# Kernel tuning notes

Measured on AMD Instinct MI355X. Metric: run time of the kernel, lower is better.

## Reference

```python
import jax, jax.numpy as jnp
import numpy as np


def setup_inputs() -> dict:
    key = jax.random.key(0)
    k_in, k_w = jax.random.split(key)
    input = jax.random.normal(k_in, (16, 64, 64, 512), dtype=jnp.float32)
    weight = jax.random.normal(k_w, (512, 512), dtype=jnp.float32)
    return {"input": input, "weight": weight}


def reference(input, weight):
    # Faithful to the torch source, including its quirky (weight*weight).sum(0)
    # (sum over the vocab axis -> (embed_dim,) vector, broadcast over vocab
    # columns; valid here because vocab_size == embed_dim).
    batch_dims, embed_dim = input.shape[:-1], input.shape[-1]
    x = input.reshape(-1, embed_dim)                     # (N, D)
    dists = -2.0 * jnp.einsum("nd,vd->nv", x, weight) + jnp.sum(weight * weight, axis=0)[None, :]
    idxes = jnp.argmin(dists, axis=1)                    # (N,)
    values = weight[idxes].reshape(*batch_dims, embed_dim)
    return values
```

## Files before the change

### kernel.cpp

```cpp
#include <hip/hip_runtime.h>


#define DIM   512
#define VOCAB 512
#define EPS_GAP 0.03f

typedef float f32x4 __attribute__((ext_vector_type(4)));
typedef short bf16x8 __attribute__((ext_vector_type(8)));
typedef unsigned long long u64;

__device__ inline unsigned short f2bf(float f){
    unsigned u = __float_as_uint(f);
    return (unsigned short)((u + 0x7fffu + ((u >> 16) & 1u)) >> 16);
}
__device__ inline float bf2f(unsigned short h){
    return __uint_as_float(((unsigned)h) << 16);
}
__device__ inline u64 packkey(float s, int v){
    unsigned u = __float_as_uint(s);
    u = (u & 0x80000000u) ? ~u : (u | 0x80000000u);
    return (((u64)u) << 32) | (unsigned)(~v);
}
__device__ inline float keyscore(u64 k){
    unsigned e = (unsigned)(k >> 32);
    return __uint_as_float((e & 0x80000000u) ? (e & 0x7fffffffu) : ~e);
}
__device__ inline int keyv(u64 k){ return (int)(~(unsigned)(k & 0xffffffffu)); }
__device__ inline u64 umax64(u64 a, u64 b){ return a > b ? a : b; }
__device__ inline u64 umin64(u64 a, u64 b){ return a < b ? a : b; }

__device__ inline void gload_lds16(const void* g, void* l){
    __builtin_amdgcn_global_load_lds(
        (const __attribute__((address_space(1))) unsigned*)g,
        (__attribute__((address_space(3))) unsigned*)l, 16, 0, 0);
}

__global__ void colsumsq_kernel(const float* __restrict__ w, float* __restrict__ c){
    const int v = blockIdx.x;
    const int lane = threadIdx.x;
    double s = 0.0;
    for (int i = lane; i < DIM; i += 64){
        const float wv = w[i * VOCAB + v];
        s += (double)wv * (double)wv;
    }
    #pragma unroll
    for (int m = 1; m <= 32; m <<= 1) s += __shfl_xor(s, m, 64);
    if (lane == 0) c[v] = (float)s;
}

__global__ void prep_w(const float* __restrict__ w,
                       unsigned short* __restrict__ whc,
                       unsigned short* __restrict__ wlc,
                       unsigned* __restrict__ cnt){
    const int i = blockIdx.x * 256 + threadIdx.x;
    const float f = w[i];
    const unsigned short h = f2bf(f);
    const unsigned short l = f2bf(f - bf2f(h));
    const int v = i >> 9, k = i & 511;
    const int d = (k >> 5) * 16384 + ((k >> 3) & 3) * 4096 + v * 8 + (k & 7);
    whc[d] = h; wlc[d] = l;
    if (i == 0) *cnt = 0u;
}

__launch_bounds__(256, 2)
__global__ void k1_scores(const float* __restrict__ x,
                          const unsigned short* __restrict__ whc,
                          const unsigned short* __restrict__ wlc,
                          const float* __restrict__ cg,
                          const float* __restrict__ w,
                          float* __restrict__ out,
                          int* __restrict__ list,
                          unsigned* __restrict__ cnt){
    __shared__ __align__(16) unsigned short Bh[16384];
    __shared__ __align__(16) unsigned short Bl[16384];
    __shared__ __align__(16) unsigned short Ah[2048];
    __shared__ __align__(16) unsigned short Al[2048];
    __shared__ u64 mergeK[64][4][2];
    __shared__ int idx_s[64];

    const int t = threadIdx.x;
    const int lane = t & 63, wv = t >> 6, quad = lane >> 4, lm = lane & 15;
    const int cb = wv << 7;
    const long rbase = (long)blockIdx.x * 64;
    const float* xblk = x + rbase * DIM;

    f32x4 acc[4][8];
    #pragma unroll
    for (int ct = 0; ct < 8; ++ct){
        const float bias = -0.5f * cg[cb + ct * 16 + lm];
        f32x4 z; z[0] = bias; z[1] = bias; z[2] = bias; z[3] = bias;
        #pragma unroll
        for (int rt = 0; rt < 4; ++rt) acc[rt][ct] = z;
    }

    for (int ch = 0; ch < 16; ++ch){
        __syncthreads();
        {
            const unsigned short* srcH = whc + ch * 16384 + (wv << 12);
            const unsigned short* srcL = wlc + ch * 16384 + (wv << 12);
            #pragma unroll
            for (int i = 0; i < 8; ++i){
                gload_lds16(srcH + i * 512 + lane * 8, &Bh[(wv << 12) + i * 512]);
                gload_lds16(srcL + i * 512 + lane * 8, &Bl[(wv << 12) + i * 512]);
            }
        }
        #pragma unroll
        for (int i = 0; i < 2; ++i){
            const int j = i * 256 + t;
            const int row = j >> 3, kq = j & 7;
            const float4 a4 = *(const float4*)(xblk + (long)row * DIM + ch * 32 + kq * 4);
            ushort4 h4, l4;
            h4.x = f2bf(a4.x); l4.x = f2bf(a4.x - bf2f(h4.x));
            h4.y = f2bf(a4.y); l4.y = f2bf(a4.y - bf2f(h4.y));
            h4.z = f2bf(a4.z); l4.z = f2bf(a4.z - bf2f(h4.z));
            h4.w = f2bf(a4.w); l4.w = f2bf(a4.w - bf2f(h4.w));
            const int d = (kq >> 1) * 512 + row * 8 + (kq & 1) * 4;
            *(ushort4*)&Ah[d] = h4;
            *(ushort4*)&Al[d] = l4;
        }
        __syncthreads();

        bf16x8 ah[4], al[4];
        #pragma unroll
        for (int rt = 0; rt < 4; ++rt){
            ah[rt] = *(const bf16x8*)&Ah[quad * 512 + (rt * 16 + lm) * 8];
            al[rt] = *(const bf16x8*)&Al[quad * 512 + (rt * 16 + lm) * 8];
        }
        #pragma unroll
        for (int ct = 0; ct < 8; ++ct){
            const int vo = quad * 4096 + (cb + ct * 16 + lm) * 8;
            const bf16x8 bh = *(const bf16x8*)&Bh[vo];
            const bf16x8 bl = *(const bf16x8*)&Bl[vo];
            #pragma unroll
            for (int rt = 0; rt < 4; ++rt){
                f32x4 a = acc[rt][ct];
                a = __builtin_amdgcn_mfma_f32_16x16x32_bf16(ah[rt], bh, a, 0, 0, 0);
                a = __builtin_amdgcn_mfma_f32_16x16x32_bf16(al[rt], bh, a, 0, 0, 0);
                a = __builtin_amdgcn_mfma_f32_16x16x32_bf16(ah[rt], bl, a, 0, 0, 0);
                acc[rt][ct] = a;
            }
        }
    }

    #pragma unroll
    for (int rt = 0; rt < 4; ++rt){
        #pragma unroll
        for (int reg = 0; reg < 4; ++reg){
            u64 b1 = 0, b2 = 0;
            #pragma unroll
            for (int ct = 0; ct < 8; ++ct){
                const u64 key = packkey(acc[rt][ct][reg], cb + ct * 16 + lm);
                if (key > b1){ b2 = b1; b1 = key; }
                else if (key > b2){ b2 = key; }
            }
            #pragma unroll
            for (int m = 1; m <= 8; m <<= 1){
                const u64 o1 = __shfl_xor(b1, m, 64);
                const u64 o2 = __shfl_xor(b2, m, 64);
                const u64 n1 = umax64(b1, o1);
                b2 = umax64(umin64(b1, o1), umax64(b2, o2));
                b1 = n1;
            }
            if (lm == 0){
                const int row = rt * 16 + quad * 4 + reg;
                mergeK[row][wv][0] = b1;
                mergeK[row][wv][1] = b2;
            }
        }
    }
    __syncthreads();
    if (t < 64){
        u64 p1 = mergeK[t][0][0], p2 = mergeK[t][0][1];
        #pragma unroll
        for (int i = 1; i < 4; ++i){
            const u64 q1 = mergeK[t][i][0], q2 = mergeK[t][i][1];
            const u64 n1 = umax64(p1, q1);
            p2 = umax64(umin64(p1, q1), umax64(p2, q2));
            p1 = n1;
        }
        idx_s[t] = keyv(p1);
        if (keyscore(p1) - keyscore(p2) < EPS_GAP){
            const unsigned p = atomicAdd(cnt, 1u);
            list[p] = (int)(rbase + t);
        }
    }
    __syncthreads();

    for (int rr = 0; rr < 64; rr += 2){
        const int row  = rr + (t >> 7);
        const int col  = (t & 127) << 2;
        const int vidx = idx_s[row];
        const float4 val = *(const float4*)(w + (long)vidx * DIM + col);
        *(float4*)(out + (rbase + row) * DIM + col) = val;
    }
}

__global__ void refine_rows(const float* __restrict__ x, const float* __restrict__ w,
                            const float* __restrict__ cg, const int* __restrict__ list,
                            const unsigned* __restrict__ cnt, float* __restrict__ out){
    __shared__ float xs[DIM];
    __shared__ u64 wk[4];
    __shared__ int bestv_s;
    const int t = threadIdx.x;
    const int n = (int)*cnt;
    for (int i = blockIdx.x; i < n; i += gridDim.x){
        const int row = list[i];
        __syncthreads();
        if (t < 128) *(float4*)&xs[t * 4] = *(const float4*)(x + (long)row * DIM + t * 4);
        __syncthreads();
        u64 best = 0;
        #pragma unroll
        for (int vv = 0; vv < 2; ++vv){
            const int v = t + vv * 256;
            const float* wr = w + (long)v * DIM;
            float s = 0.f;
            for (int k = 0; k < DIM; k += 4){
                const float4 w4 = *(const float4*)(wr + k);
                s = fmaf(w4.x, xs[k + 0], s);
                s = fmaf(w4.y, xs[k + 1], s);
                s = fmaf(w4.z, xs[k + 2], s);
                s = fmaf(w4.w, xs[k + 3], s);
            }
            s -= 0.5f * cg[v];
            best = umax64(best, packkey(s, v));
        }
        #pragma unroll
        for (int m = 1; m <= 32; m <<= 1) best = umax64(best, __shfl_xor(best, m, 64));
        if ((t & 63) == 0) wk[t >> 6] = best;
        __syncthreads();
        if (t == 0){
            const u64 b = umax64(umax64(wk[0], wk[1]), umax64(wk[2], wk[3]));
            bestv_s = keyv(b);
        }
        __syncthreads();
        const int bv = bestv_s;
        if (t < 128)
            *(float4*)(out + (long)row * DIM + t * 4) =
                *(const float4*)(w + (long)bv * DIM + t * 4);
    }
}

__launch_bounds__(256)
__global__ void fallback_full(const float* __restrict__ x, const float* __restrict__ w,
                              float* __restrict__ out){
    __shared__ __align__(16) float As[16][68];
    __shared__ __align__(16) float Bs[16][VOCAB];
    __shared__ int   idx_sf[64];
    __shared__ float c_s[VOCAB];

    const int t  = threadIdx.x;
    const int tx = t & 31;
    const int ty = t >> 5;
    const long rbase = (long)blockIdx.x * 64;
    const float* xblk = x + rbase * DIM;

    for (int vv = t; vv < VOCAB; vv += 256){
        double s = 0.0;
        for (int i = 0; i < DIM; ++i){
            const float wvv = w[i * VOCAB + vv];
            s += (double)wvv * (double)wvv;
        }
        c_s[vv] = (float)s;
    }

    float acc[8][16];
    #pragma unroll
    for (int r = 0; r < 8; ++r)
        #pragma unroll
        for (int j = 0; j < 16; ++j) acc[r][j] = 0.0f;

    for (int k0 = 0; k0 < DIM; k0 += 16){
        __syncthreads();
        {
            const int r  = t >> 2;
            const int kq = (t & 3) << 2;
            const float4 a4 = *(const float4*)(xblk + (long)r * DIM + k0 + kq);
            As[kq + 0][r] = a4.x; As[kq + 1][r] = a4.y;
            As[kq + 2][r] = a4.z; As[kq + 3][r] = a4.w;
        }
        #pragma unroll
        for (int vb = 0; vb < 8; ++vb){
            const int v  = (t >> 2) + (vb << 6);
            const int kq = (t & 3) << 2;
            const float4 b4 = *(const float4*)(w + (long)v * DIM + k0 + kq);
            Bs[kq + 0][v] = b4.x; Bs[kq + 1][v] = b4.y;
            Bs[kq + 2][v] = b4.z; Bs[kq + 3][v] = b4.w;
        }
        __syncthreads();

        #pragma unroll
        for (int k = 0; k < 16; ++k){
            float a[8];
            const float4 a03 = *(const float4*)&As[k][ty * 8];
            const float4 a47 = *(const float4*)&As[k][ty * 8 + 4];
            a[0] = a03.x; a[1] = a03.y; a[2] = a03.z; a[3] = a03.w;
            a[4] = a47.x; a[5] = a47.y; a[6] = a47.z; a[7] = a47.w;
            float b[16];
            #pragma unroll
            for (int j = 0; j < 16; ++j) b[j] = Bs[k][tx + (j << 5)];
            #pragma unroll
            for (int r = 0; r < 8; ++r)
                #pragma unroll
                for (int j = 0; j < 16; ++j)
                    acc[r][j] = fmaf(a[r], b[j], acc[r][j]);
        }
    }

    #pragma unroll
    for (int r = 0; r < 8; ++r){
        float best = acc[r][0] - 0.5f * c_s[tx];
        int   bv   = tx;
        #pragma unroll
        for (int j = 1; j < 16; ++j){
            const float s = acc[r][j] - 0.5f * c_s[tx + (j << 5)];
            if (s > best){ best = s; bv = tx + (j << 5); }
        }
        unsigned u = __float_as_uint(best);
        u = (u & 0x80000000u) ? ~u : (u | 0x80000000u);
        u64 key = ((u64)u << 32) | (unsigned)(~(unsigned)bv);
        #pragma unroll
        for (int m = 1; m <= 16; m <<= 1){
            const u64 o = __shfl_xor(key, m, 64);
            if (o > key) key = o;
        }
        if (tx == 0) idx_sf[ty * 8 + r] = (int)(~(unsigned)(key & 0xFFFFFFFFull));
    }
    __syncthreads();

    for (int rr = 0; rr < 64; rr += 2){
        const int row  = rr + (t >> 7);
        const int col  = (t & 127) << 2;
        const int vidx = idx_sf[row];
        const float4 val = *(const float4*)(w + (long)vidx * DIM + col);
        *(float4*)(out + (rbase + row) * DIM + col) = val;
    }
}

extern "C" void kernel_launch(void* const* d_in, const int* in_sizes, int n_in,
                              void* d_out, int out_size, void* d_ws, size_t ws_size,
                              hipStream_t stream){
    const float* x = (const float*)d_in[0];
    const float* w = (const float*)d_in[1];
    float* out = (float*)d_out;
    const int rows = in_sizes[0] / DIM;

    const size_t whc_off  = 0;
    const size_t wlc_off  = whc_off + (size_t)DIM * VOCAB * 2;
    const size_t c_off    = wlc_off + (size_t)DIM * VOCAB * 2;
    const size_t list_off = c_off   + (size_t)VOCAB * 4;
    const size_t cnt_off  = list_off + (size_t)rows * 4;
    const size_t need     = cnt_off + 16;

    if (ws_size >= need){
        unsigned short* whc = (unsigned short*)((char*)d_ws + whc_off);
        unsigned short* wlc = (unsigned short*)((char*)d_ws + wlc_off);
        float*    c    = (float*)((char*)d_ws + c_off);
        int*      list = (int*)((char*)d_ws + list_off);
        unsigned* cnt  = (unsigned*)((char*)d_ws + cnt_off);

        prep_w<<<(DIM * VOCAB) / 256, 256, 0, stream>>>(w, whc, wlc, cnt);
        colsumsq_kernel<<<VOCAB, 64, 0, stream>>>(w, c);
        k1_scores<<<rows / 64, 256, 0, stream>>>(x, whc, wlc, c, w, out, list, cnt);
        refine_rows<<<512, 256, 0, stream>>>(x, w, c, list, cnt, out);
    } else {
        fallback_full<<<rows / 64, 256, 0, stream>>>(x, w, out);
    }
}
```

Before: 341.1 us.

## Read weight fragments directly from global memory and stage larger input tiles in LDS

Weight bf16 hi/lo fragments are no longer staged through LDS with global_load_lds. Each wave now loads its own B fragments straight from global memory, where they should mostly hit in L2. The A tile is staged in two halves of 256 columns instead of sixteen 32-column chunks, which cuts the number of block barriers from 32 to 4. The cost is more global and L2 traffic per MFMA step and exposed load latency, since there is no double buffering. Part of this is offset by fewer synchronisations and less LDS use.

```diff
diff --git a/kernel.cpp b/kernel.cpp
--- a/kernel.cpp
+++ b/kernel.cpp
@@ -28,12 +28,6 @@
 __device__ inline int keyv(u64 k){ return (int)(~(unsigned)(k & 0xffffffffu)); }
 __device__ inline u64 umax64(u64 a, u64 b){ return a > b ? a : b; }
 __device__ inline u64 umin64(u64 a, u64 b){ return a < b ? a : b; }
-
-__device__ inline void gload_lds16(const void* g, void* l){
-    __builtin_amdgcn_global_load_lds(
-        (const __attribute__((address_space(1))) unsigned*)g,
-        (__attribute__((address_space(3))) unsigned*)l, 16, 0, 0);
-}
 
 __global__ void colsumsq_kernel(const float* __restrict__ w, float* __restrict__ c){
     const int v = blockIdx.x;
@@ -71,10 +65,8 @@
                           float* __restrict__ out,
                           int* __restrict__ list,
                           unsigned* __restrict__ cnt){
-    __shared__ __align__(16) unsigned short Bh[16384];
-    __shared__ __align__(16) unsigned short Bl[16384];
-    __shared__ __align__(16) unsigned short Ah[2048];
-    __shared__ __align__(16) unsigned short Al[2048];
+    __shared__ __align__(16) unsigned short Ah[16384];
+    __shared__ __align__(16) unsigned short Al[16384];
     __shared__ u64 mergeK[64][4][2];
     __shared__ int idx_s[64];
 
@@ -93,51 +85,50 @@
         for (int rt = 0; rt < 4; ++rt) acc[rt][ct] = z;
     }
 
-    for (int ch = 0; ch < 16; ++ch){
-        __syncthreads();
-        {
-            const unsigned short* srcH = whc + ch * 16384 + (wv << 12);
-            const unsigned short* srcL = wlc + ch * 16384 + (wv << 12);
-            #pragma unroll
-            for (int i = 0; i < 8; ++i){
-                gload_lds16(srcH + i * 512 + lane * 8, &Bh[(wv << 12) + i * 512]);
-                gload_lds16(srcL + i * 512 + lane * 8, &Bl[(wv << 12) + i * 512]);
-            }
-        }
-        #pragma unroll
-        for (int i = 0; i < 2; ++i){
-            const int j = i * 256 + t;
-            const int row = j >> 3, kq = j & 7;
-            const float4 a4 = *(const float4*)(xblk + (long)row * DIM + ch * 32 + kq * 4);
+    for (int half = 0; half < 2; ++half){
+        __syncthreads();
+        #pragma unroll 8
+        for (int jj = 0; jj < 16; ++jj){
+            const int j   = jj * 256 + t;
+            const int row = (j >> 3) & 63;
+            const int k4  = (j & 7) | ((j >> 9) << 3);
+            const int kk  = k4 << 2;
+            const float4 a4 = *(const float4*)(xblk + (long)row * DIM + half * 256 + kk);
             ushort4 h4, l4;
             h4.x = f2bf(a4.x); l4.x = f2bf(a4.x - bf2f(h4.x));
             h4.y = f2bf(a4.y); l4.y = f2bf(a4.y - bf2f(h4.y));
             h4.z = f2bf(a4.z); l4.z = f2bf(a4.z - bf2f(h4.z));
             h4.w = f2bf(a4.w); l4.w = f2bf(a4.w - bf2f(h4.w));
-            const int d = (kq >> 1) * 512 + row * 8 + (kq & 1) * 4;
+            const int d = (((kk >> 5) * 4 + ((kk >> 3) & 3)) * 64 + row) * 8 + (kk & 7);
             *(ushort4*)&Ah[d] = h4;
             *(ushort4*)&Al[d] = l4;
         }
         __syncthreads();
 
-        bf16x8 ah[4], al[4];
-        #pragma unroll
-        for (int rt = 0; rt < 4; ++rt){
-            ah[rt] = *(const bf16x8*)&Ah[quad * 512 + (rt * 16 + lm) * 8];
-            al[rt] = *(const bf16x8*)&Al[quad * 512 + (rt * 16 + lm) * 8];
-        }
-        #pragma unroll
-        for (int ct = 0; ct < 8; ++ct){
-            const int vo = quad * 4096 + (cb + ct * 16 + lm) * 8;
-            const bf16x8 bh = *(const bf16x8*)&Bh[vo];
-            const bf16x8 bl = *(const bf16x8*)&Bl[vo];
+        for (int ch2 = 0; ch2 < 8; ++ch2){
+            const int ch = half * 8 + ch2;
+            bf16x8 ah[4], al[4];
             #pragma unroll
             for (int rt = 0; rt < 4; ++rt){
-                f32x4 a = acc[rt][ct];
-                a = __builtin_amdgcn_mfma_f32_16x16x32_bf16(ah[rt], bh, a, 0, 0, 0);
-                a = __builtin_amdgcn_mfma_f32_16x16x32_bf16(al[rt], bh, a, 0, 0, 0);
-                a = __builtin_amdgcn_mfma_f32_16x16x32_bf16(ah[rt], bl, a, 0, 0, 0);
-                acc[rt][ct] = a;
+                const int d = ((ch2 * 4 + quad) * 64 + rt * 16 + lm) * 8;
+                ah[rt] = *(const bf16x8*)&Ah[d];
+                al[rt] = *(const bf16x8*)&Al[d];
+            }
+            const unsigned short* bbh = whc + ch * 16384 + quad * 4096;
+            const unsigned short* bbl = wlc + ch * 16384 + quad * 4096;
+            #pragma unroll
+            for (int ct = 0; ct < 8; ++ct){
+                const int co = (cb + ct * 16 + lm) * 8;
+                const bf16x8 bh = *(const bf16x8*)(bbh + co);
+                const bf16x8 bl = *(const bf16x8*)(bbl + co);
+                #pragma unroll
+                for (int rt = 0; rt < 4; ++rt){
+                    f32x4 a = acc[rt][ct];
+                    a = __builtin_amdgcn_mfma_f32_16x16x32_bf16(ah[rt], bh, a, 0, 0, 0);
+                    a = __builtin_amdgcn_mfma_f32_16x16x32_bf16(al[rt], bh, a, 0, 0, 0);
+                    a = __builtin_amdgcn_mfma_f32_16x16x32_bf16(ah[rt], bl, a, 0, 0, 0);
+                    acc[rt][ct] = a;
+                }
             }
         }
     }
```

New measurement: 355.8 us. 1.04x slower.
